# Kernel optimization log

Measured on AMD Instinct MI355X. Metric: run time of the kernel, lower is better.

The kernel has to match this reference:

```python
import jax, jax.numpy as jnp
import numpy as np

B, S, D, H = 16, 4096, 1024, 1024
VOCAB = 512
EMB_DIM = 3


def setup_inputs() -> dict:
    key = jax.random.key(0)
    ks = jax.random.split(key, 12)
    sd = 1.0 / np.sqrt(D)
    sh = 1.0 / np.sqrt(H)
    return {
        "hs": jax.random.normal(ks[0], (B, S, D), dtype=jnp.float32),
        "ht_k": jax.random.normal(ks[1], (B, D), dtype=jnp.float32),
        "hm_k": jax.random.normal(ks[2], (B, H), dtype=jnp.float32),
        "Ws_w": jax.random.uniform(ks[3], (H, D), jnp.float32, -sd, sd),
        "Ws_b": jax.random.uniform(ks[4], (H,), jnp.float32, -sd, sd),
        "Wt_w": jax.random.uniform(ks[5], (H, D), jnp.float32, -sd, sd),
        "Wt_b": jax.random.uniform(ks[6], (H,), jnp.float32, -sd, sd),
        "Wr_w": jax.random.uniform(ks[7], (H, H), jnp.float32, -sh, sh),
        "Wr_b": jax.random.uniform(ks[8], (H,), jnp.float32, -sh, sh),
        "We_w": jax.random.uniform(ks[9], (H,), jnp.float32, -sh, sh),
        "We_b": jax.random.uniform(ks[10], (1,), jnp.float32, -sh, sh),
        "emb_table": jax.random.normal(ks[11], (VOCAB * VOCAB, EMB_DIM), dtype=jnp.float32),
        "entity_lambda": jnp.array([0.3, 0.5, 0.2], dtype=jnp.float32),
        "hs_i": jax.random.randint(jax.random.fold_in(key, 100), (B, S), 0, VOCAB),
        "ht_k_i": jax.random.randint(jax.random.fold_in(key, 101), (B,), 0, VOCAB),
    }


def reference(hs, ht_k, hm_k, Ws_w, Ws_b, Wt_w, Wt_b, Wr_w, Wr_b, We_w, We_b,
              emb_table, entity_lambda, hs_i, ht_k_i):
    # Projections
    W_hs = jnp.einsum('bsd,hd->bsh', hs, Ws_w) + Ws_b          # [B,S,H]
    W_ht = (ht_k @ Wt_w.T + Wt_b)[:, None, :]                   # [B,1,H]
    W_hm = (hm_k @ Wr_w.T + Wr_b)[:, None, :]                   # [B,1,H]
    # Additive attention score
    W_sum = jnp.tanh(W_hs + W_ht + W_hm) @ We_w + We_b[0]       # [B,S]
    # Relative-position bias: gather then contract with lambda
    rel_pos = hs_i * VOCAB + ht_k_i[:, None]                    # [B,S]
    rel_value = emb_table[rel_pos] @ entity_lambda              # [B,S]
    W_sum = W_sum + rel_value
    # Softmax over sequence, weighted sum of projected source states
    W_softmax = jax.nn.softmax(W_sum, axis=1)                   # [B,S]
    alpha = jnp.einsum('bs,bsh->bh', W_softmax, W_hs)           # [B,H]
    return alpha
```

## Files before the change

### kernel.cpp

```cpp
#include <hip/hip_runtime.h>
#include <hip/hip_bf16.h>
#include <cstdint>
#include <cstddef>

typedef __attribute__((ext_vector_type(4))) float f32x4;
typedef __attribute__((ext_vector_type(8))) short short8;

#define S_LEN 4096
#define D_DIM 1024
#define H_DIM 1024
#define B_SZ  16
#define M_TOT (B_SZ * S_LEN)

__device__ __forceinline__ unsigned short f2bf(float f) {
  unsigned int u = __float_as_uint(f);
  u += 0x7fffu + ((u >> 16) & 1u);
  return (unsigned short)(u >> 16);
}

__device__ __forceinline__ void gload_lds16(void* lds, const void* g) {
  __builtin_amdgcn_global_load_lds(
      (const __attribute__((address_space(1))) unsigned int*)g,
      (__attribute__((address_space(3))) unsigned int*)lds, 16, 0, 0);
}

__device__ __forceinline__ float tanh_fast(float x) {
  return 1.0f - 2.0f / (1.0f + __expf(2.0f * x));
}

__global__ void cvt_hs_kernel(const float* __restrict__ w,
                              unsigned short* __restrict__ o) {
  size_t i = ((size_t)blockIdx.x * 256 + threadIdx.x) * 8;
  float4 v0 = *(const float4*)(w + i);
  float4 v1 = *(const float4*)(w + i + 4);
  union { unsigned short us[8]; short8 v; } pk;
  pk.us[0] = f2bf(v0.x); pk.us[1] = f2bf(v0.y);
  pk.us[2] = f2bf(v0.z); pk.us[3] = f2bf(v0.w);
  pk.us[4] = f2bf(v1.x); pk.us[5] = f2bf(v1.y);
  pk.us[6] = f2bf(v1.z); pk.us[7] = f2bf(v1.w);
  *(short8*)(o + i) = pk.v;
}

__global__ void cvt_w_kernel(const float* __restrict__ w,
                             unsigned short* __restrict__ o) {
  int i = (blockIdx.x * 256 + threadIdx.x) * 8;
  float4 v0 = *(const float4*)(w + i);
  float4 v1 = *(const float4*)(w + i + 4);
  union { unsigned short us[8]; short8 v; } pk;
  pk.us[0] = f2bf(v0.x); pk.us[1] = f2bf(v0.y);
  pk.us[2] = f2bf(v0.z); pk.us[3] = f2bf(v0.w);
  pk.us[4] = f2bf(v1.x); pk.us[5] = f2bf(v1.y);
  pk.us[6] = f2bf(v1.z); pk.us[7] = f2bf(v1.w);
  *(short8*)(o + i) = pk.v;
}

__global__ void prep_c_kernel(const float* __restrict__ ht,
                              const float* __restrict__ hm,
                              const float* __restrict__ Wt_w,
                              const float* __restrict__ Wt_b,
                              const float* __restrict__ Wr_w,
                              const float* __restrict__ Wr_b,
                              float* __restrict__ cvec) {
  int gw = blockIdx.x * 4 + (threadIdx.x >> 6);
  int lane = threadIdx.x & 63;
  int b = gw >> 10;
  int h = gw & 1023;
  const float* a1 = ht + b * D_DIM;
  const float* w1 = Wt_w + (size_t)h * D_DIM;
  const float* a2 = hm + b * H_DIM;
  const float* w2 = Wr_w + (size_t)h * H_DIM;
  float acc = 0.f;
#pragma unroll
  for (int i = 0; i < 4; ++i) {
    int d = lane * 4 + i * 256;
    float4 x1 = *(const float4*)(a1 + d);
    float4 y1 = *(const float4*)(w1 + d);
    float4 x2 = *(const float4*)(a2 + d);
    float4 y2 = *(const float4*)(w2 + d);
    acc += x1.x * y1.x + x1.y * y1.y + x1.z * y1.z + x1.w * y1.w;
    acc += x2.x * y2.x + x2.y * y2.y + x2.z * y2.z + x2.w * y2.w;
  }
#pragma unroll
  for (int off = 32; off >= 1; off >>= 1) acc += __shfl_xor(acc, off);
  if (lane == 0) cvec[b * H_DIM + h] = acc + Wt_b[h] + Wr_b[h];
}

__global__ __launch_bounds__(256, 4) void score_gemm9_kernel(
    const unsigned short* __restrict__ hsb,
    const unsigned short* __restrict__ Wsb,
    const float* __restrict__ cvec,
    const float* __restrict__ We_w,
    float* __restrict__ score_part) {
  __shared__ __align__(16) unsigned short lA[8192];
  __shared__ __align__(16) unsigned short lB[8192];
  __shared__ float scorebuf[2][128];

  const int tid = threadIdx.x;
  const int lane = tid & 63;
  const int wave = tid >> 6;
  const int wr = wave >> 1;
  const int wc = wave & 1;
  const int l15 = lane & 15;
  const int lg = lane >> 4;

  int dd = blockIdx.x;
  int tileid = (dd & 7) * 512 + (dd >> 3);
  const int mtile = tileid >> 3;
  const int nc = tileid & 7;
  const int m0 = mtile * 128;
  const int n0 = nc * 128;
  const int b = m0 >> 12;

  const int r0 = tid >> 3;
  const int sl = tid & 7;
  const int c0 = ((sl ^ (r0 & 7)) << 3);
  const unsigned short* pA = hsb + (size_t)(m0 + r0) * D_DIM + c0;
  const unsigned short* pB = Wsb + (size_t)(n0 + r0) * D_DIM + c0;
  const int dst = tid * 8;

  const int arow = wr * 64 + l15;
  const int brow = wc * 64 + l15;
  const int swz0 = ((lg ^ (l15 & 7)) << 3);
  const int swz1 = (((4 + lg) ^ (l15 & 7)) << 3);
  const int aoff0 = arow * 64 + swz0;
  const int aoff1 = arow * 64 + swz1;
  const int boff0 = brow * 64 + swz0;
  const int boff1 = brow * 64 + swz1;

  f32x4 acc[4][4];
#pragma unroll
  for (int i = 0; i < 4; ++i)
#pragma unroll
    for (int j = 0; j < 4; ++j) acc[i][j] = (f32x4){0.f, 0.f, 0.f, 0.f};

#pragma unroll
  for (int s = 0; s < 16; ++s) {
    const int KO = s * 64;
#pragma unroll
    for (int i = 0; i < 4; ++i)
      gload_lds16(&lA[dst + i * 2048], pA + (size_t)i * 32768 + KO);
#pragma unroll
    for (int i = 0; i < 4; ++i)
      gload_lds16(&lB[dst + i * 2048], pB + (size_t)i * 32768 + KO);
    __syncthreads();
    short8 fa[4], fb[4];
#pragma unroll
    for (int ni = 0; ni < 4; ++ni)
      fb[ni] = *(const short8*)(lB + boff0 + ni * 1024);
#pragma unroll
    for (int mi = 0; mi < 4; ++mi)
      fa[mi] = *(const short8*)(lA + aoff0 + mi * 1024);
#pragma unroll
    for (int mi = 0; mi < 4; ++mi)
#pragma unroll
      for (int ni = 0; ni < 4; ++ni)
        acc[mi][ni] = __builtin_amdgcn_mfma_f32_16x16x32_bf16(
            fa[mi], fb[ni], acc[mi][ni], 0, 0, 0);
#pragma unroll
    for (int ni = 0; ni < 4; ++ni)
      fb[ni] = *(const short8*)(lB + boff1 + ni * 1024);
#pragma unroll
    for (int mi = 0; mi < 4; ++mi)
      fa[mi] = *(const short8*)(lA + aoff1 + mi * 1024);
#pragma unroll
    for (int mi = 0; mi < 4; ++mi)
#pragma unroll
      for (int ni = 0; ni < 4; ++ni)
        acc[mi][ni] = __builtin_amdgcn_mfma_f32_16x16x32_bf16(
            fa[mi], fb[ni], acc[mi][ni], 0, 0, 0);
    __syncthreads();
  }

  float chv[4], whv[4];
#pragma unroll
  for (int ni = 0; ni < 4; ++ni) {
    int h = n0 + wc * 64 + ni * 16 + l15;
    chv[ni] = cvec[b * H_DIM + h];
    whv[ni] = We_w[h];
  }
#pragma unroll
  for (int mi = 0; mi < 4; ++mi)
#pragma unroll
    for (int r = 0; r < 4; ++r) {
      float s = 0.f;
#pragma unroll
      for (int ni = 0; ni < 4; ++ni)
        s += tanh_fast(acc[mi][ni][r] + chv[ni]) * whv[ni];
      s += __shfl_xor(s, 1);
      s += __shfl_xor(s, 2);
      s += __shfl_xor(s, 4);
      s += __shfl_xor(s, 8);
      if (l15 == 0) scorebuf[wc][wr * 64 + mi * 16 + lg * 4 + r] = s;
    }
  __syncthreads();
  if (tid < 128) {
    score_part[(size_t)nc * M_TOT + m0 + tid] =
        scorebuf[0][tid] + scorebuf[1][tid];
  }
}

__global__ __launch_bounds__(256) void score_gemm_fp32_kernel(
    const float* __restrict__ hs,
    const unsigned short* __restrict__ Wsb,
    const float* __restrict__ cvec,
    const float* __restrict__ We_w,
    float* __restrict__ score_part) {
  __shared__ __align__(16) unsigned short lA[128 * 64];
  __shared__ __align__(16) unsigned short lB[128 * 64];
  __shared__ float scorebuf[2][128];

  const int tid = threadIdx.x;
  const int lane = tid & 63;
  const int wave = tid >> 6;
  const int wr = wave >> 1;
  const int wc = wave & 1;
  const int mtile = blockIdx.x;
  const int gy = blockIdx.y;
  const int m0 = mtile * 128;
  const int b = mtile >> 5;
  const int l15 = lane & 15;
  const int lg = lane >> 4;

  float rowsum[4][4];
#pragma unroll
  for (int i = 0; i < 4; ++i)
#pragma unroll
    for (int j = 0; j < 4; ++j) rowsum[i][j] = 0.f;

  for (int ncq = gy * 4; ncq < gy * 4 + 4; ++ncq) {
    const int n0 = ncq * 128;
    f32x4 acc[4][4];
#pragma unroll
    for (int i = 0; i < 4; ++i)
#pragma unroll
      for (int j = 0; j < 4; ++j) acc[i][j] = (f32x4){0.f, 0.f, 0.f, 0.f};

    for (int k0 = 0; k0 < D_DIM; k0 += 64) {
#pragma unroll
      for (int r = 0; r < 4; ++r) {
        int s = tid + r * 256;
        int row = s >> 3, slx = s & 7;
        int src = slx ^ (row & 7);
        gload_lds16(&lB[s * 8], Wsb + (size_t)(n0 + row) * D_DIM + k0 + src * 8);
      }
      float4 a0[4], a1[4];
#pragma unroll
      for (int r = 0; r < 4; ++r) {
        int s = tid + r * 256;
        int row = s >> 3, slx = s & 7;
        int src = slx ^ (row & 7);
        const float* ga = hs + (size_t)(m0 + row) * D_DIM + k0 + src * 8;
        a0[r] = *(const float4*)ga;
        a1[r] = *(const float4*)(ga + 4);
      }
#pragma unroll
      for (int r = 0; r < 4; ++r) {
        int s = tid + r * 256;
        union { unsigned short us[8]; short8 v; } pk;
        pk.us[0] = f2bf(a0[r].x); pk.us[1] = f2bf(a0[r].y);
        pk.us[2] = f2bf(a0[r].z); pk.us[3] = f2bf(a0[r].w);
        pk.us[4] = f2bf(a1[r].x); pk.us[5] = f2bf(a1[r].y);
        pk.us[6] = f2bf(a1[r].z); pk.us[7] = f2bf(a1[r].w);
        *(short8*)(&lA[s * 8]) = pk.v;
      }
      __syncthreads();
#pragma unroll
      for (int kf = 0; kf < 2; ++kf) {
        short8 af[4], bfr[4];
        int cgrp = kf * 4 + lg;
#pragma unroll
        for (int mi = 0; mi < 4; ++mi) {
          int row = wr * 64 + mi * 16 + l15;
          af[mi] = *(const short8*)&lA[row * 64 + (cgrp ^ (row & 7)) * 8];
        }
#pragma unroll
        for (int ni = 0; ni < 4; ++ni) {
          int row = wc * 64 + ni * 16 + l15;
          bfr[ni] = *(const short8*)&lB[row * 64 + (cgrp ^ (row & 7)) * 8];
        }
#pragma unroll
        for (int mi = 0; mi < 4; ++mi)
#pragma unroll
          for (int ni = 0; ni < 4; ++ni)
            acc[mi][ni] = __builtin_amdgcn_mfma_f32_16x16x32_bf16(
                af[mi], bfr[ni], acc[mi][ni], 0, 0, 0);
      }
      __syncthreads();
    }
#pragma unroll
    for (int ni = 0; ni < 4; ++ni) {
      int h = n0 + wc * 64 + ni * 16 + l15;
      float ch = cvec[b * H_DIM + h];
      float wh = We_w[h];
#pragma unroll
      for (int mi = 0; mi < 4; ++mi)
#pragma unroll
        for (int r2 = 0; r2 < 4; ++r2)
          rowsum[mi][r2] += tanh_fast(acc[mi][ni][r2] + ch) * wh;
    }
  }
#pragma unroll
  for (int mi = 0; mi < 4; ++mi)
#pragma unroll
    for (int r2 = 0; r2 < 4; ++r2) {
      float v = rowsum[mi][r2];
      v += __shfl_xor(v, 1);
      v += __shfl_xor(v, 2);
      v += __shfl_xor(v, 4);
      v += __shfl_xor(v, 8);
      rowsum[mi][r2] = v;
    }
  if (l15 == 0) {
#pragma unroll
    for (int mi = 0; mi < 4; ++mi)
#pragma unroll
      for (int r2 = 0; r2 < 4; ++r2)
        scorebuf[wc][wr * 64 + mi * 16 + lg * 4 + r2] = rowsum[mi][r2];
  }
  __syncthreads();
  if (tid < 128) {
    score_part[(size_t)gy * M_TOT + m0 + tid] =
        scorebuf[0][tid] + scorebuf[1][tid];
  }
}

template <int NP>
__global__ void softmax_kernel(const float* __restrict__ part,
                               const int* __restrict__ hs_i,
                               const int* __restrict__ ht_i,
                               const float* __restrict__ emb,
                               const float* __restrict__ lam,
                               float* __restrict__ wout) {
  int b = blockIdx.x;
  int tid = threadIdx.x;
  float lam0 = lam[0], lam1 = lam[1], lam2 = lam[2];
  int tk = ht_i[b];
  float xs[16];
  float mx = -1e30f;
#pragma unroll
  for (int i = 0; i < 16; ++i) {
    int s = tid + i * 256;
    size_t m = (size_t)b * S_LEN + s;
    float x = 0.f;
#pragma unroll
    for (int g = 0; g < NP; ++g) x += part[(size_t)g * M_TOT + m];
    int idx = hs_i[m] * 512 + tk;
    const float* e = emb + (size_t)idx * 3;
    x += e[0] * lam0 + e[1] * lam1 + e[2] * lam2;
    xs[i] = x;
    mx = fmaxf(mx, x);
  }
  __shared__ float redm[4];
  __shared__ float reds[4];
#pragma unroll
  for (int off = 32; off >= 1; off >>= 1) mx = fmaxf(mx, __shfl_xor(mx, off));
  if ((tid & 63) == 0) redm[tid >> 6] = mx;
  __syncthreads();
  mx = fmaxf(fmaxf(redm[0], redm[1]), fmaxf(redm[2], redm[3]));
  float sum = 0.f;
#pragma unroll
  for (int i = 0; i < 16; ++i) {
    xs[i] = __expf(xs[i] - mx);
    sum += xs[i];
  }
#pragma unroll
  for (int off = 32; off >= 1; off >>= 1) sum += __shfl_xor(sum, off);
  if ((tid & 63) == 0) reds[tid >> 6] = sum;
  __syncthreads();
  sum = reds[0] + reds[1] + reds[2] + reds[3];
  float inv = 1.0f / sum;
#pragma unroll
  for (int i = 0; i < 16; ++i)
    wout[(size_t)b * S_LEN + tid + i * 256] = xs[i] * inv;
}

__global__ void wsum_bf16_kernel(const unsigned short* __restrict__ hsb,
                                 const float* __restrict__ w,
                                 float* __restrict__ u) {
  int bx = blockIdx.x;
  int b = bx >> 5;
  int sc = bx & 31;
  int tid = threadIdx.x;
  int dcol = tid * 4;
  int s0 = sc * 128;
  const unsigned short* base = hsb + ((size_t)b * S_LEN + s0) * D_DIM + dcol;
  const float* wrow = w + (size_t)b * S_LEN + s0;
  float4 acc = {0.f, 0.f, 0.f, 0.f};
#pragma unroll 4
  for (int i = 0; i < 128; ++i) {
    float ww = wrow[i];
    ushort2 v01 = *(const ushort2*)(base + (size_t)i * D_DIM);
    ushort2 v23 = *(const ushort2*)(base + (size_t)i * D_DIM + 2);
    acc.x += ww * __uint_as_float((unsigned int)v01.x << 16);
    acc.y += ww * __uint_as_float((unsigned int)v01.y << 16);
    acc.z += ww * __uint_as_float((unsigned int)v23.x << 16);
    acc.w += ww * __uint_as_float((unsigned int)v23.y << 16);
  }
  atomicAdd(&u[b * D_DIM + dcol + 0], acc.x);
  atomicAdd(&u[b * D_DIM + dcol + 1], acc.y);
  atomicAdd(&u[b * D_DIM + dcol + 2], acc.z);
  atomicAdd(&u[b * D_DIM + dcol + 3], acc.w);
}

__global__ void wsum_kernel(const float* __restrict__ hs,
                            const float* __restrict__ w,
                            float* __restrict__ u) {
  int bx = blockIdx.x;
  int b = bx >> 5;
  int sc = bx & 31;
  int tid = threadIdx.x;
  int dcol = tid * 4;
  int s0 = sc * 128;
  const float* base = hs + ((size_t)b * S_LEN + s0) * D_DIM + dcol;
  const float* wrow = w + (size_t)b * S_LEN + s0;
  float4 acc = {0.f, 0.f, 0.f, 0.f};
#pragma unroll 4
  for (int i = 0; i < 128; ++i) {
    float ww = wrow[i];
    float4 v = *(const float4*)(base + (size_t)i * D_DIM);
    acc.x += ww * v.x;
    acc.y += ww * v.y;
    acc.z += ww * v.z;
    acc.w += ww * v.w;
  }
  atomicAdd(&u[b * D_DIM + dcol + 0], acc.x);
  atomicAdd(&u[b * D_DIM + dcol + 1], acc.y);
  atomicAdd(&u[b * D_DIM + dcol + 2], acc.z);
  atomicAdd(&u[b * D_DIM + dcol + 3], acc.w);
}

__global__ void alpha_kernel(const float* __restrict__ u,
                             const float* __restrict__ Ws_w,
                             const float* __restrict__ Ws_b,
                             float* __restrict__ out) {
  int gw = blockIdx.x * 4 + (threadIdx.x >> 6);
  int lane = threadIdx.x & 63;
  int b = gw >> 10;
  int h = gw & 1023;
  const float* ur = u + b * D_DIM;
  const float* wrow = Ws_w + (size_t)h * D_DIM;
  float acc = 0.f;
#pragma unroll
  for (int i = 0; i < 4; ++i) {
    int dcol = lane * 4 + i * 256;
    float4 x = *(const float4*)(ur + dcol);
    float4 y = *(const float4*)(wrow + dcol);
    acc += x.x * y.x + x.y * y.y + x.z * y.z + x.w * y.w;
  }
#pragma unroll
  for (int off = 32; off >= 1; off >>= 1) acc += __shfl_xor(acc, off);
  if (lane == 0) out[b * H_DIM + h] = acc + Ws_b[h];
}

extern "C" void kernel_launch(void* const* d_in, const int* in_sizes, int n_in,
                              void* d_out, int out_size, void* d_ws,
                              size_t ws_size, hipStream_t stream) {
  const float* hs = (const float*)d_in[0];
  const float* ht_k = (const float*)d_in[1];
  const float* hm_k = (const float*)d_in[2];
  const float* Ws_w = (const float*)d_in[3];
  const float* Ws_b = (const float*)d_in[4];
  const float* Wt_w = (const float*)d_in[5];
  const float* Wt_b = (const float*)d_in[6];
  const float* Wr_w = (const float*)d_in[7];
  const float* Wr_b = (const float*)d_in[8];
  const float* We_w = (const float*)d_in[9];
  const float* emb = (const float*)d_in[11];
  const float* lam = (const float*)d_in[12];
  const int* hs_i = (const int*)d_in[13];
  const int* ht_i = (const int*)d_in[14];
  float* out = (float*)d_out;

  const size_t HSB = (size_t)M_TOT * D_DIM * 2;
  const size_t FAST_NEEDED =
      HSB + 2097152 + 2097152 + 262144 + 65536 + 65536;

  char* ws = (char*)d_ws;
  if (ws_size >= FAST_NEEDED) {
    unsigned short* hsb = (unsigned short*)ws;
    unsigned short* Wsb = (unsigned short*)(ws + HSB);
    float* part = (float*)(ws + HSB + 2097152);
    float* wgt = (float*)(ws + HSB + 2097152 + 2097152);
    float* u = (float*)(ws + HSB + 2097152 + 2097152 + 262144);
    float* cvec = (float*)(ws + HSB + 2097152 + 2097152 + 262144 + 65536);

    cvt_hs_kernel<<<32768, 256, 0, stream>>>(hs, hsb);
    cvt_w_kernel<<<512, 256, 0, stream>>>(Ws_w, Wsb);
    prep_c_kernel<<<4096, 256, 0, stream>>>(ht_k, hm_k, Wt_w, Wt_b, Wr_w,
                                            Wr_b, cvec);
    score_gemm9_kernel<<<4096, 256, 0, stream>>>(hsb, Wsb, cvec, We_w, part);
    softmax_kernel<8><<<16, 256, 0, stream>>>(part, hs_i, ht_i, emb, lam, wgt);
    hipMemsetAsync(u, 0, B_SZ * D_DIM * sizeof(float), stream);
    wsum_bf16_kernel<<<512, 256, 0, stream>>>(hsb, wgt, u);
    alpha_kernel<<<4096, 256, 0, stream>>>(u, Ws_w, Ws_b, out);
    return;
  }

  unsigned short* Wsb = (unsigned short*)(ws);
  float* cvec = (float*)(ws + 2097152);
  float* part = (float*)(ws + 2097152 + 65536);
  float* wgt = (float*)(ws + 2097152 + 65536 + 524288);
  float* u = (float*)(ws + 2097152 + 65536 + 524288 + 262144);

  cvt_w_kernel<<<512, 256, 0, stream>>>(Ws_w, Wsb);
  prep_c_kernel<<<4096, 256, 0, stream>>>(ht_k, hm_k, Wt_w, Wt_b, Wr_w, Wr_b,
                                          cvec);
  dim3 g2(512, 2);
  score_gemm_fp32_kernel<<<g2, 256, 0, stream>>>(hs, Wsb, cvec, We_w, part);
  softmax_kernel<2><<<16, 256, 0, stream>>>(part, hs_i, ht_i, emb, lam, wgt);
  hipMemsetAsync(u, 0, B_SZ * D_DIM * sizeof(float), stream);
  wsum_kernel<<<512, 256, 0, stream>>>(hs, wgt, u);
  alpha_kernel<<<4096, 256, 0, stream>>>(u, Ws_w, Ws_b, out);
}
```

Measured before the change: 284.8 us.

## Enlarge score GEMM to 256x256 tiles with double-buffered pipelined LDS loads

The bf16 score GEMM moves from 128x128 tiles with 256 threads to 256x256 tiles with 512 threads (8 waves). Operands are staged in a 128KB dynamic-LDS double buffer, and the next K-slice's global-to-LDS loads are interleaved between MFMA quarter-blocks using explicit waitcnt, barriers and setprio. The aim is more operand reuse per byte loaded and less load latency exposed at the old per-iteration syncthreads. In exchange there are fewer blocks, one block per CU given the LDS size, higher register pressure, and four score partials per row, so the softmax template is switched to 4.

```diff
diff --git a/kernel.cpp b/kernel.cpp
--- a/kernel.cpp
+++ b/kernel.cpp
@@ -85,30 +85,31 @@
   if (lane == 0) cvec[b * H_DIM + h] = acc + Wt_b[h] + Wr_b[h];
 }
 
-__global__ __launch_bounds__(256, 4) void score_gemm9_kernel(
+__global__ __launch_bounds__(512, 2) void score_gemm10_kernel(
     const unsigned short* __restrict__ hsb,
     const unsigned short* __restrict__ Wsb,
     const float* __restrict__ cvec,
     const float* __restrict__ We_w,
     float* __restrict__ score_part) {
-  __shared__ __align__(16) unsigned short lA[8192];
-  __shared__ __align__(16) unsigned short lB[8192];
-  __shared__ float scorebuf[2][128];
+  extern __shared__ unsigned short dynls[];
+  unsigned short* lA = dynls;
+  unsigned short* lB = dynls + 32768;
+  __shared__ float scorebuf[4][256];
 
   const int tid = threadIdx.x;
   const int lane = tid & 63;
   const int wave = tid >> 6;
-  const int wr = wave >> 1;
-  const int wc = wave & 1;
+  const int wm = wave >> 2;
+  const int wn = wave & 3;
   const int l15 = lane & 15;
   const int lg = lane >> 4;
 
   int dd = blockIdx.x;
-  int tileid = (dd & 7) * 512 + (dd >> 3);
-  const int mtile = tileid >> 3;
-  const int nc = tileid & 7;
-  const int m0 = mtile * 128;
-  const int n0 = nc * 128;
+  int tileid = (dd & 7) * 128 + (dd >> 3);
+  const int mtile = tileid >> 2;
+  const int nc = tileid & 3;
+  const int m0 = mtile * 256;
+  const int n0 = nc * 256;
   const int b = m0 >> 12;
 
   const int r0 = tid >> 3;
@@ -116,70 +117,151 @@
   const int c0 = ((sl ^ (r0 & 7)) << 3);
   const unsigned short* pA = hsb + (size_t)(m0 + r0) * D_DIM + c0;
   const unsigned short* pB = Wsb + (size_t)(n0 + r0) * D_DIM + c0;
-  const int dst = tid * 8;
-
-  const int arow = wr * 64 + l15;
-  const int brow = wc * 64 + l15;
+  const int dst0 = tid * 8;
+  const int dst1 = 4096 + tid * 8;
+
+#define STG_A0(T)                                                     \
+  do {                                                                \
+    gload_lds16(lA + ((T)&1) * 16384 + dst0, pA + (T) * 64);          \
+    gload_lds16(lA + ((T)&1) * 16384 + dst1, pA + 65536 + (T) * 64);  \
+  } while (0)
+#define STG_A1(T)                                                     \
+  do {                                                                \
+    gload_lds16(lA + ((T)&1) * 16384 + 8192 + dst0,                   \
+                pA + 131072 + (T) * 64);                              \
+    gload_lds16(lA + ((T)&1) * 16384 + 8192 + dst1,                   \
+                pA + 131072 + 65536 + (T) * 64);                      \
+  } while (0)
+#define STG_B0(T)                                                     \
+  do {                                                                \
+    gload_lds16(lB + ((T)&1) * 16384 + dst0, pB + (T) * 64);          \
+    gload_lds16(lB + ((T)&1) * 16384 + dst1, pB + 65536 + (T) * 64);  \
+  } while (0)
+#define STG_B1(T)                                                     \
+  do {                                                                \
+    gload_lds16(lB + ((T)&1) * 16384 + 8192 + dst0,                   \
+                pB + 131072 + (T) * 64);                              \
+    gload_lds16(lB + ((T)&1) * 16384 + 8192 + dst1,                   \
+                pB + 131072 + 65536 + (T) * 64);                      \
+  } while (0)
+
   const int swz0 = ((lg ^ (l15 & 7)) << 3);
   const int swz1 = (((4 + lg) ^ (l15 & 7)) << 3);
-  const int aoff0 = arow * 64 + swz0;
-  const int aoff1 = arow * 64 + swz1;
-  const int boff0 = brow * 64 + swz0;
-  const int boff1 = brow * 64 + swz1;
-
-  f32x4 acc[4][4];
-#pragma unroll
-  for (int i = 0; i < 4; ++i)
+  const int afix = wm * 8192 + l15 * 64;
+  const int bfix = (wn >> 1) * 8192 + ((wn & 1) * 64 + l15) * 64;
+
+  f32x4 acc[8][4];
+#pragma unroll
+  for (int i = 0; i < 8; ++i)
 #pragma unroll
     for (int j = 0; j < 4; ++j) acc[i][j] = (f32x4){0.f, 0.f, 0.f, 0.f};
 
-#pragma unroll
-  for (int s = 0; s < 16; ++s) {
-    const int KO = s * 64;
-#pragma unroll
-    for (int i = 0; i < 4; ++i)
-      gload_lds16(&lA[dst + i * 2048], pA + (size_t)i * 32768 + KO);
-#pragma unroll
-    for (int i = 0; i < 4; ++i)
-      gload_lds16(&lB[dst + i * 2048], pB + (size_t)i * 32768 + KO);
-    __syncthreads();
-    short8 fa[4], fb[4];
-#pragma unroll
-    for (int ni = 0; ni < 4; ++ni)
-      fb[ni] = *(const short8*)(lB + boff0 + ni * 1024);
-#pragma unroll
-    for (int mi = 0; mi < 4; ++mi)
-      fa[mi] = *(const short8*)(lA + aoff0 + mi * 1024);
-#pragma unroll
-    for (int mi = 0; mi < 4; ++mi)
-#pragma unroll
-      for (int ni = 0; ni < 4; ++ni)
-        acc[mi][ni] = __builtin_amdgcn_mfma_f32_16x16x32_bf16(
-            fa[mi], fb[ni], acc[mi][ni], 0, 0, 0);
-#pragma unroll
-    for (int ni = 0; ni < 4; ++ni)
-      fb[ni] = *(const short8*)(lB + boff1 + ni * 1024);
-#pragma unroll
-    for (int mi = 0; mi < 4; ++mi)
-      fa[mi] = *(const short8*)(lA + aoff1 + mi * 1024);
-#pragma unroll
-    for (int mi = 0; mi < 4; ++mi)
-#pragma unroll
-      for (int ni = 0; ni < 4; ++ni)
-        acc[mi][ni] = __builtin_amdgcn_mfma_f32_16x16x32_bf16(
-            fa[mi], fb[ni], acc[mi][ni], 0, 0, 0);
-    __syncthreads();
-  }
+#define BAR() __builtin_amdgcn_s_barrier()
+#define VM(N) asm volatile("s_waitcnt vmcnt(" #N ")" ::: "memory")
+
+#define MM16(ACB, FA, FB)                                                  \
+  {                                                                        \
+    __builtin_amdgcn_s_setprio(1);                                         \
+    _Pragma("unroll") for (int kk = 0; kk < 2; ++kk) {                     \
+      _Pragma("unroll") for (int mi = 0; mi < 4; ++mi) {                   \
+        _Pragma("unroll") for (int ni = 0; ni < 2; ++ni) {                 \
+          ACB = __builtin_amdgcn_mfma_f32_16x16x32_bf16(                   \
+              FA[kk * 4 + mi], FB[kk * 2 + ni], ACB, 0, 0, 0);             \
+        }                                                                  \
+      }                                                                    \
+    }                                                                      \
+    __builtin_amdgcn_s_setprio(0);                                         \
+  }
+
+#define TILE(T, S0, S1, S2, S3, WQ)                                        \
+  {                                                                        \
+    short8 fa_lo[8], fa_hi[8], fb_lo[4], fb_hi[4];                         \
+                                                                   \
+    _Pragma("unroll") for (int kk = 0; kk < 2; ++kk) {                     \
+      const int sw = kk ? swz1 : swz0;                                     \
+      _Pragma("unroll") for (int mi = 0; mi < 4; ++mi)                     \
+          fa_lo[kk * 4 + mi] = *(const short8*)(lA + ((T)&1) * 16384 +     \
+                                                afix + mi * 1024 + sw);    \
+      _Pragma("unroll") for (int ni = 0; ni < 2; ++ni)                     \
+          fb_lo[kk * 2 + ni] = *(const short8*)(lB + ((T)&1) * 16384 +     \
+                                                bfix + ni * 1024 + sw);    \
+    }                                                                      \
+    S0;                                                                    \
+    BAR();                                                                 \
+    MM16(acc[mi][ni], fa_lo, fb_lo);                                       \
+    BAR();                                                                 \
+                                                                   \
+    _Pragma("unroll") for (int kk = 0; kk < 2; ++kk) {                     \
+      const int sw = kk ? swz1 : swz0;                                     \
+      _Pragma("unroll") for (int mi = 0; mi < 4; ++mi)                     \
+          fa_hi[kk * 4 + mi] = *(const short8*)(lA + ((T)&1) * 16384 +     \
+                                                afix + 4096 + mi * 1024 +  \
+                                                sw);                       \
+    }                                                                      \
+    S1;                                                                    \
+    BAR();                                                                 \
+    MM16(acc[4 + mi][ni], fa_hi, fb_lo);                                   \
+    BAR();                                                                 \
+                                                                   \
+    _Pragma("unroll") for (int kk = 0; kk < 2; ++kk) {                     \
+      const int sw = kk ? swz1 : swz0;                                     \
+      _Pragma("unroll") for (int ni = 0; ni < 2; ++ni)                     \
+          fb_hi[kk * 2 + ni] = *(const short8*)(lB + ((T)&1) * 16384 +     \
+                                                bfix + 2048 + ni * 1024 +  \
+                                                sw);                       \
+    }                                                                      \
+    S2;                                                                    \
+    BAR();                                                                 \
+    MM16(acc[4 + mi][2 + ni], fa_hi, fb_hi);                               \
+    BAR();                                                                 \
+                                                                   \
+    S3;                                                                    \
+    BAR();                                                                 \
+    MM16(acc[mi][2 + ni], fa_lo, fb_hi);                                   \
+    WQ;                                                                    \
+    BAR();                                                                 \
+  }
+
+  STG_A0(0); STG_A1(0); STG_B0(0); STG_B1(0);
+  STG_A0(1); STG_A1(1);
+  VM(4);
+  BAR();
+
+  TILE(0, STG_B0(1), STG_B1(1), STG_A0(2), STG_A1(2), VM(4))
+  TILE(1, STG_B0(2), STG_B1(2), STG_A0(3), STG_A1(3), VM(4))
+  TILE(2, STG_B0(3), STG_B1(3), STG_A0(4), STG_A1(4), VM(4))
+  TILE(3, STG_B0(4), STG_B1(4), STG_A0(5), STG_A1(5), VM(4))
+  TILE(4, STG_B0(5), STG_B1(5), STG_A0(6), STG_A1(6), VM(4))
+  TILE(5, STG_B0(6), STG_B1(6), STG_A0(7), STG_A1(7), VM(4))
+  TILE(6, STG_B0(7), STG_B1(7), STG_A0(8), STG_A1(8), VM(4))
+  TILE(7, STG_B0(8), STG_B1(8), STG_A0(9), STG_A1(9), VM(4))
+  TILE(8, STG_B0(9), STG_B1(9), STG_A0(10), STG_A1(10), VM(4))
+  TILE(9, STG_B0(10), STG_B1(10), STG_A0(11), STG_A1(11), VM(4))
+  TILE(10, STG_B0(11), STG_B1(11), STG_A0(12), STG_A1(12), VM(4))
+  TILE(11, STG_B0(12), STG_B1(12), STG_A0(13), STG_A1(13), VM(4))
+  TILE(12, STG_B0(13), STG_B1(13), STG_A0(14), STG_A1(14), VM(4))
+  TILE(13, STG_B0(14), STG_B1(14), STG_A0(15), STG_A1(15), VM(4))
+  TILE(14, STG_B0(15), STG_B1(15), , , VM(0))
+  TILE(15, , , , , )
+
+#undef TILE
+#undef MM16
+#undef STG_A0
+#undef STG_A1
+#undef STG_B0
+#undef STG_B1
+#undef VM
+#undef BAR
 
   float chv[4], whv[4];
 #pragma unroll
   for (int ni = 0; ni < 4; ++ni) {
-    int h = n0 + wc * 64 + ni * 16 + l15;
+    int h = n0 + wn * 64 + ni * 16 + l15;
     chv[ni] = cvec[b * H_DIM + h];
     whv[ni] = We_w[h];
   }
 #pragma unroll
-  for (int mi = 0; mi < 4; ++mi)
+  for (int mi = 0; mi < 8; ++mi)
 #pragma unroll
     for (int r = 0; r < 4; ++r) {
       float s = 0.f;
@@ -190,12 +272,13 @@
       s += __shfl_xor(s, 2);
       s += __shfl_xor(s, 4);
       s += __shfl_xor(s, 8);
-      if (l15 == 0) scorebuf[wc][wr * 64 + mi * 16 + lg * 4 + r] = s;
+      if (l15 == 0) scorebuf[wn][wm * 128 + mi * 16 + lg * 4 + r] = s;
     }
   __syncthreads();
-  if (tid < 128) {
-    score_part[(size_t)nc * M_TOT + m0 + tid] =
-        scorebuf[0][tid] + scorebuf[1][tid];
+  if (tid < 256) {
+    float s = scorebuf[0][tid] + scorebuf[1][tid] + scorebuf[2][tid] +
+              scorebuf[3][tid];
+    score_part[(size_t)nc * M_TOT + m0 + tid] = s;
   }
 }
 
@@ -484,12 +567,16 @@
     float* u = (float*)(ws + HSB + 2097152 + 2097152 + 262144);
     float* cvec = (float*)(ws + HSB + 2097152 + 2097152 + 262144 + 65536);
 
+    hipFuncSetAttribute((const void*)score_gemm10_kernel,
+                        hipFuncAttributeMaxDynamicSharedMemorySize, 131072);
+
     cvt_hs_kernel<<<32768, 256, 0, stream>>>(hs, hsb);
     cvt_w_kernel<<<512, 256, 0, stream>>>(Ws_w, Wsb);
     prep_c_kernel<<<4096, 256, 0, stream>>>(ht_k, hm_k, Wt_w, Wt_b, Wr_w,
                                             Wr_b, cvec);
-    score_gemm9_kernel<<<4096, 256, 0, stream>>>(hsb, Wsb, cvec, We_w, part);
-    softmax_kernel<8><<<16, 256, 0, stream>>>(part, hs_i, ht_i, emb, lam, wgt);
+    score_gemm10_kernel<<<1024, 512, 131072, stream>>>(hsb, Wsb, cvec, We_w,
+                                                       part);
+    softmax_kernel<4><<<16, 256, 0, stream>>>(part, hs_i, ht_i, emb, lam, wgt);
     hipMemsetAsync(u, 0, B_SZ * D_DIM * sizeof(float), stream);
     wsum_bf16_kernel<<<512, 256, 0, stream>>>(hsb, wgt, u);
     alpha_kernel<<<4096, 256, 0, stream>>>(u, Ws_w, Ws_b, out);
```

Result: faster. 270.5 us (-5.0%).
